# Kernel tuning notes

Measured on AMD Instinct MI355X. Metric: run time of the kernel, lower is better.

Reference implementation:

```python
import jax, jax.numpy as jnp
import numpy as np

V, E, U = 32000, 256, 512  # vocab, embed dim, LSTM units
B, S = 16, 130             # batch, seq len


def lstm_layer(x, mask, k, r, b):
    """Keras LSTMCell semantics. x:[B,T,D], mask:[B,T]; gates order i,f,c,o."""
    h0 = jnp.zeros((x.shape[0], U), x.dtype)
    c0 = h0
    xs = jnp.swapaxes(x, 0, 1)      # [T,B,D]
    ms = jnp.swapaxes(mask, 0, 1)   # [T,B]

    def step(carry, inp):
        h, c = carry
        xt, mt = inp
        z = xt @ k + h @ r + b
        i, f, g, o = jnp.split(z, 4, axis=-1)
        i = jax.nn.sigmoid(i); f = jax.nn.sigmoid(f); o = jax.nn.sigmoid(o)
        cn = f * c + i * jnp.tanh(g)
        hn = o * jnp.tanh(cn)
        m = mt[:, None]
        hn = jnp.where(m, hn, h)  # masked steps carry previous state/output
        cn = jnp.where(m, cn, c)
        return (hn, cn), hn

    _, ys = jax.lax.scan(step, (h0, c0), (xs, ms))
    return jnp.swapaxes(ys, 0, 1)  # [B,T,U]


def stacked_lstm(x, mask, params):
    h = x
    for (k, r, b) in params:
        h = lstm_layer(h, mask, k, r, b)
    return h


def setup_inputs() -> dict:
    key = jax.random.key(0)
    ks = jax.random.split(key, 20)
    d = {}
    d["seqs"] = jax.random.randint(ks[0], (B, S), 0, V)
    d["emb"] = jax.random.normal(ks[1], (V, E), jnp.float32) * 0.01
    i = 2
    for pre in ("f", "b"):
        in_dims = [E, U]
        for l in range(2):
            d[f"{pre}k{l}"] = jax.random.normal(ks[i], (in_dims[l], 4 * U), jnp.float32) * 0.05; i += 1
            d[f"{pre}r{l}"] = jax.random.normal(ks[i], (U, 4 * U), jnp.float32) * 0.05; i += 1
            d[f"{pre}b{l}"] = jnp.zeros((4 * U,), jnp.float32)
    d["Wp"] = jax.random.normal(ks[i], (2 * U, V), jnp.float32) * 0.02
    d["bp"] = jnp.zeros((V,), jnp.float32)
    return d


def reference(seqs, emb, fk0, fr0, fb0, fk1, fr1, fb1, bk0, br0, bb0, bk1, br1, bb1, Wp, bp):
    mask = seqs != 0                 # mask_zero=True
    embedded = emb[seqs]             # [B,S,E]
    # forward LM over tokens 0..S-2
    f = stacked_lstm(embedded[:, :-1], mask[:, :-1], [(fk0, fr0, fb0), (fk1, fr1, fb1)])
    # backward LM over tokens 1..S-1 (go_backwards: scan reversed input)
    xb = embedded[:, 1:][:, ::-1]
    mb = mask[:, 1:][:, ::-1]
    b = stacked_lstm(xb, mb, [(bk0, br0, bb0), (bk1, br1, bb1)])
    b_rev = b[:, ::-1]               # tf.reverse -> chronological order
    o = jnp.concatenate([f[:, :-1], b_rev[:, 1:]], axis=-1)  # [B,S-2,2U]
    return o @ Wp + bp               # [B,S-2,V]
```

## Files before the change

kernel.cpp:

```cpp
#include <hip/hip_runtime.h>

typedef __attribute__((ext_vector_type(8))) short bf16x8;
typedef __attribute__((ext_vector_type(4))) float f32x4;

__device__ __forceinline__ unsigned short f2bf(float x){
  union { float f; unsigned u; } v; v.f = x;
  unsigned r = v.u + 0x7FFFu + ((v.u >> 16) & 1u);
  return (unsigned short)(r >> 16);
}

__device__ __forceinline__ float sigm(float x){
  return 1.f / (1.f + __builtin_amdgcn_exp2f(-1.44269504f * x));
}
__device__ __forceinline__ float tanhfast(float x){
  return 2.f / (1.f + __builtin_amdgcn_exp2f(-2.88539008f * x)) - 1.f;
}

#define BYPASS_ST_SHORT(base, val) \
  asm volatile("global_store_short %0, %1, off sc0 sc1" :: "v"(base), "v"(val))

__device__ __forceinline__ int ld_flag(const int* p){
  int v;
  asm volatile("global_load_dword %0, %1, off sc0 sc1\n\t"
               "s_waitcnt vmcnt(0)"
               : "=v"(v) : "v"(p) : "memory");
  return v;
}

__device__ __forceinline__ void gload_lds16(const void* g, void* l){
  __builtin_amdgcn_global_load_lds(
      (const __attribute__((address_space(1))) unsigned*)g,
      (__attribute__((address_space(3))) unsigned*)l, 16, 0, 0);
}

__global__ void embed_kernel(const int* __restrict__ seqs, const float* __restrict__ emb,
                             unsigned short* __restrict__ x, int* __restrict__ mask,
                             int* __restrict__ flags){
  const int t = blockIdx.x, b = blockIdx.y, l = threadIdx.x;
  if (t == 0 && b == 0){
    #pragma unroll
    for (int j = 0; j < 16; ++j) flags[l + j*64] = 0;
  }
  const int tok = seqs[b*130 + t];
  if (l == 0) mask[b*130 + t] = (tok != 0) ? 1 : 0;
  const float* src = emb + (size_t)tok * 256;
  unsigned short* dst = x + ((size_t)b*130 + t)*256;
  #pragma unroll
  for (int j = 0; j < 4; ++j) dst[l + j*64] = f2bf(src[l + j*64]);
}

__global__ __launch_bounds__(512) void prep_transpose(
    const float* __restrict__ Wp,  unsigned short* __restrict__ WpT,
    const float* __restrict__ fk0, unsigned short* __restrict__ fk0T,
    const float* __restrict__ fr0, unsigned short* __restrict__ fr0T,
    const float* __restrict__ fk1, unsigned short* __restrict__ fk1T,
    const float* __restrict__ fr1, unsigned short* __restrict__ fr1T,
    const float* __restrict__ bk0, unsigned short* __restrict__ bk0T,
    const float* __restrict__ br0, unsigned short* __restrict__ br0T,
    const float* __restrict__ bk1, unsigned short* __restrict__ bk1T,
    const float* __restrict__ br1, unsigned short* __restrict__ br1T)
{
  __shared__ float tf[32*65];
  const int tid = threadIdx.x;
  const int tx = tid & 63, ty = tid >> 6;
  const int orow = tid & 31, oc = tid >> 5;
  for (int tile = blockIdx.x; tile < 19584; tile += gridDim.x){
    const float* src; unsigned short* dst; int R, C, r0, c0;
    if (tile < 16000){
      src = Wp; dst = WpT; R = 1024; C = 32000;
      const int kt = tile / 500, nt = tile - kt*500;
      r0 = kt*32; c0 = nt*64;
    } else {
      int u = tile - 16000;
      C = 2048;
      if (u < 256)      { src = fk0; dst = fk0T; R = 256;           }
      else if (u < 768) { src = fr0; dst = fr0T; R = 512; u -= 256; }
      else if (u < 1280){ src = fk1; dst = fk1T; R = 512; u -= 768; }
      else if (u < 1792){ src = fr1; dst = fr1T; R = 512; u -= 1280;}
      else if (u < 2048){ src = bk0; dst = bk0T; R = 256; u -= 1792;}
      else if (u < 2560){ src = br0; dst = br0T; R = 512; u -= 2048;}
      else if (u < 3072){ src = bk1; dst = bk1T; R = 512; u -= 2560;}
      else              { src = br1; dst = br1T; R = 512; u -= 3072;}
      const int kt = u >> 5, nt = u & 31;
      r0 = kt*32; c0 = nt*64;
    }
    #pragma unroll
    for (int j = 0; j < 4; ++j)
      tf[(ty + 8*j)*65 + tx] = src[(size_t)(r0 + ty + 8*j)*C + c0 + tx];
    __syncthreads();
    #pragma unroll
    for (int j = 0; j < 4; ++j)
      dst[(size_t)(c0 + oc + 16*j)*R + r0 + orow] = f2bf(tf[orow*65 + oc + 16*j]);
    __syncthreads();
  }
}

__global__ __launch_bounds__(512, 2) void lstm_coop(
    const unsigned short* __restrict__ x, const int* __restrict__ maskg,
    const unsigned short* __restrict__ fk0T, const unsigned short* __restrict__ fr0T,
    const unsigned short* __restrict__ fk1T, const unsigned short* __restrict__ fr1T,
    const unsigned short* __restrict__ bk0T, const unsigned short* __restrict__ br0T,
    const unsigned short* __restrict__ bk1T, const unsigned short* __restrict__ br1T,
    const float* __restrict__ fb0, const float* __restrict__ fb1,
    const float* __restrict__ bb0, const float* __restrict__ bb1,
    unsigned short* h0f, unsigned short* h0b,
    unsigned short* aproj, int* flags)
{
  const int wg = blockIdx.x;
  const int dir = wg >> 5;
  const int layer = (wg >> 4) & 1;
  const int u0 = (wg & 15) * 32;
  const int tid = threadIdx.x;
  const int w = tid >> 6, l = tid & 63;
  const int gate = w >> 1, half = w & 1;
  const int lr = l & 15, lk = l >> 4;
  const int cglob = gate*512 + u0 + half*16 + lr;

  const unsigned short* kT = (layer == 0) ? (dir ? bk0T : fk0T) : (dir ? bk1T : fk1T);
  const unsigned short* rT = (layer == 0) ? (dir ? br0T : fr0T) : (dir ? br1T : fr1T);
  const float* bias = (layer == 0) ? (dir ? bb0 : fb0) : (dir ? bb1 : fb1);
  unsigned short* h0 = dir ? h0b : h0f;

  int* fown  = flags + (layer*2 + dir)*256;
  int* fprod = flags + dir*256;
  int* fself = fown + (wg & 15)*16;

  bf16x8 wreg[16], kreg[16];
  #pragma unroll
  for (int i = 0; i < 16; ++i)
    wreg[i] = *(const bf16x8*)(rT + (size_t)cglob*512 + i*32 + lk*8);
  if (layer == 0){
    #pragma unroll
    for (int i = 0; i < 8; ++i)
      kreg[i] = *(const bf16x8*)(kT + (size_t)cglob*256 + i*32 + lk*8);
  } else {
    #pragma unroll
    for (int i = 0; i < 16; ++i)
      kreg[i] = *(const bf16x8*)(kT + (size_t)cglob*512 + i*32 + lk*8);
  }

  __shared__ float z_lds[4][16][32];
  __shared__ int mask_s[16*130];
  __shared__ __attribute__((aligned(16))) char h_lds[16*1024];
  __shared__ __attribute__((aligned(16))) char h2_lds[16*1024];
  for (int i = tid; i < 16*130; i += 512) mask_s[i] = maskg[i];

  float c_reg = 0.f, h_reg = 0.f;
  const int gu = tid & 31, gb = tid >> 5;
  const float bzi = bias[u0+gu], bzf = bias[512 + u0+gu];
  const float bzc = bias[1024 + u0+gu], bzo = bias[1536 + u0+gu];
  __syncthreads();

  for (int t = 0; t < 128; ++t){
    {
      const int* fp = nullptr; int tgt = 0;
      if (l < 16){ fp = fown + l*16; tgt = t; }
      else if (l < 32 && layer == 1){ fp = fprod + (l-16)*16; tgt = t + 1; }
      if (fp){
        while (ld_flag(fp) < tgt) __builtin_amdgcn_s_sleep(1);
      }
    }

    const int r0s = w*2;
    if (layer == 0){
      if (t > 0){
        #pragma unroll
        for (int j = 0; j < 2; ++j){
          const int r = r0s + j;
          const unsigned short* g = h0 + ((size_t)(t-1)*16 + r)*512 + ((l ^ (r & 7))*8);
          gload_lds16(g, h_lds + r*1024);
        }
      }
    } else {
      #pragma unroll
      for (int j = 0; j < 2; ++j){
        const int r = r0s + j;
        const unsigned short* g = h0 + ((size_t)t*16 + r)*512 + ((l ^ (r & 7))*8);
        gload_lds16(g, h_lds + r*1024);
      }
      if (t > 0){
        const int prow = dir ? (128 - t) : (t - 1);
        #pragma unroll
        for (int j = 0; j < 2; ++j){
          const int r = r0s + j;
          const unsigned short* g = aproj + ((size_t)(r*128 + prow))*1024 + dir*512 + ((l ^ (r & 7))*8);
          gload_lds16(g, h2_lds + r*1024);
        }
      }
    }

    f32x4 a0 = {0.f,0.f,0.f,0.f}, a1 = a0;
    const int fsw = (lr & 7) << 4;
    if (layer == 0){
      const int pos = dir ? (129 - t) : t;
      const unsigned short* xa = x + ((size_t)lr*130 + pos)*256 + lk*8;
      #pragma unroll
      for (int i = 0; i < 8; i += 2){
        bf16x8 va = *(const bf16x8*)(xa + i*32);
        bf16x8 vb = *(const bf16x8*)(xa + i*32 + 32);
        a0 = __builtin_amdgcn_mfma_f32_16x16x32_bf16(va, kreg[i],   a0, 0, 0, 0);
        a1 = __builtin_amdgcn_mfma_f32_16x16x32_bf16(vb, kreg[i+1], a1, 0, 0, 0);
      }
      if (t > 0){
        asm volatile("s_waitcnt vmcnt(0)" ::: "memory");
        __syncthreads();
        #pragma unroll
        for (int i = 0; i < 16; i += 2){
          bf16x8 v0 = *(const bf16x8*)(h_lds + lr*1024 + ((lk*16 + (i  )*64) ^ fsw));
          bf16x8 v1 = *(const bf16x8*)(h_lds + lr*1024 + ((lk*16 + (i+1)*64) ^ fsw));
          a0 = __builtin_amdgcn_mfma_f32_16x16x32_bf16(v0, wreg[i],   a0, 0, 0, 0);
          a1 = __builtin_amdgcn_mfma_f32_16x16x32_bf16(v1, wreg[i+1], a1, 0, 0, 0);
        }
      }
    } else {
      asm volatile("s_waitcnt vmcnt(0)" ::: "memory");
      __syncthreads();
      #pragma unroll
      for (int i = 0; i < 16; i += 2){
        bf16x8 v0 = *(const bf16x8*)(h_lds + lr*1024 + ((lk*16 + (i  )*64) ^ fsw));
        bf16x8 v1 = *(const bf16x8*)(h_lds + lr*1024 + ((lk*16 + (i+1)*64) ^ fsw));
        a0 = __builtin_amdgcn_mfma_f32_16x16x32_bf16(v0, kreg[i],   a0, 0, 0, 0);
        a1 = __builtin_amdgcn_mfma_f32_16x16x32_bf16(v1, kreg[i+1], a1, 0, 0, 0);
      }
      if (t > 0){
        #pragma unroll
        for (int i = 0; i < 16; i += 2){
          bf16x8 v0 = *(const bf16x8*)(h2_lds + lr*1024 + ((lk*16 + (i  )*64) ^ fsw));
          bf16x8 v1 = *(const bf16x8*)(h2_lds + lr*1024 + ((lk*16 + (i+1)*64) ^ fsw));
          a0 = __builtin_amdgcn_mfma_f32_16x16x32_bf16(v0, wreg[i],   a0, 0, 0, 0);
          a1 = __builtin_amdgcn_mfma_f32_16x16x32_bf16(v1, wreg[i+1], a1, 0, 0, 0);
        }
      }
    }
    {
      f32x4 acc = a0 + a1;
      #pragma unroll
      for (int r = 0; r < 4; ++r) z_lds[gate][lk*4 + r][half*16 + lr] = acc[r];
    }
    __syncthreads();

    {
      const float zi = z_lds[0][gb][gu] + bzi;
      const float zf = z_lds[1][gb][gu] + bzf;
      const float zc = z_lds[2][gb][gu] + bzc;
      const float zo = z_lds[3][gb][gu] + bzo;
      const float iv = sigm(zi);
      const float fv = sigm(zf);
      const float ov = sigm(zo);
      const float gv = tanhfast(zc);
      float cn = fv*c_reg + iv*gv;
      float hn = ov*tanhfast(cn);
      const int pos = dir ? (129 - t) : t;
      if (mask_s[gb*130 + pos] == 0){ cn = c_reg; hn = h_reg; }
      c_reg = cn; h_reg = hn;
      const unsigned short hb = f2bf(hn);
      if (layer == 0){
        unsigned short* p = h0 + ((size_t)t*16 + gb)*512 + u0 + gu;
        BYPASS_ST_SHORT(p, (unsigned)hb);
      } else {
        const int row = dir ? (127 - t) : t;
        unsigned short* p = aproj + ((size_t)gb*128 + row)*1024 + dir*512 + u0 + gu;
        BYPASS_ST_SHORT(p, (unsigned)hb);
      }
    }
    asm volatile("s_waitcnt vmcnt(0)" ::: "memory");
    __syncthreads();
    if (tid == 0){
      int v = t + 1;
      asm volatile("global_store_dword %0, %1, off sc0 sc1" :: "v"(fself), "v"(v) : "memory");
    }
  }
}

__global__ __launch_bounds__(256) void gemm_bf16(
    const unsigned short* __restrict__ A, const unsigned short* __restrict__ Bt,
    const float* __restrict__ bias, float* __restrict__ C,
    int M, int N, int K)
{
  __shared__ unsigned short lA[3][128*32], lB[3][128*32];
  const int tid = threadIdx.x;
  const int w = tid >> 6, l = tid & 63;
  const int wr = w >> 1, wc = w & 1;
  const int lr = l & 15, lk = l >> 4;
  const int orig = blockIdx.x;
  const int logical = (orig & 7)*500 + (orig >> 3);
  const int mt = logical & 15;
  const int nt = logical >> 4;
  const int brow = mt * 128, bcol = nt * 128;

  const int base0 = w*2048;
  const int base1 = w*2048 + 1024;
  const int L0 = base0 + l*16, L1 = base1 + l*16;
  const int Lg0 = L0 ^ (((L0 >> 7) & 3) << 4);
  const int Lg1 = L1 ^ (((L1 >> 7) & 3) << 4);
  const int row0 = Lg0 >> 6, kb0 = Lg0 & 63;
  const int row1 = Lg1 >> 6, kb1 = Lg1 & 63;

  f32x4 acc[4][4] = {};

  #define STAGE_KT(kt_, bu_) do{ \
    const int k0_ = (kt_) * 32; \
    gload_lds16((const char*)(A + (size_t)(brow+row0)*K + k0_) + kb0, (char*)lA[bu_] + base0); \
    gload_lds16((const char*)(Bt + (size_t)(bcol+row0)*K + k0_) + kb0, (char*)lB[bu_] + base0); \
    gload_lds16((const char*)(A + (size_t)(brow+row1)*K + k0_) + kb1, (char*)lA[bu_] + base1); \
    gload_lds16((const char*)(Bt + (size_t)(bcol+row1)*K + k0_) + kb1, (char*)lB[bu_] + base1); \
  }while(0)

  STAGE_KT(0, 0);
  STAGE_KT(1, 1);
  asm volatile("s_waitcnt vmcnt(4)" ::: "memory");
  __syncthreads();

  for (int kt = 0; kt < 32; ++kt){
    const int bu = kt - (kt / 3) * 3;
    if (kt < 30){
      const int nb = (kt + 2) - ((kt + 2) / 3) * 3;
      STAGE_KT(kt + 2, nb);
    }
    bf16x8 af[4], bfr[4];
    #pragma unroll
    for (int m = 0; m < 4; ++m){
      const int L = (wr*64 + m*16 + lr)*64 + lk*16;
      const int sp = L ^ (((L >> 7) & 3) << 4);
      af[m] = *(const bf16x8*)((char*)lA[bu] + sp);
    }
    #pragma unroll
    for (int n = 0; n < 4; ++n){
      const int L = (wc*64 + n*16 + lr)*64 + lk*16;
      const int sp = L ^ (((L >> 7) & 3) << 4);
      bfr[n] = *(const bf16x8*)((char*)lB[bu] + sp);
    }
    #pragma unroll
    for (int m = 0; m < 4; ++m)
      #pragma unroll
      for (int n = 0; n < 4; ++n)
        acc[m][n] = __builtin_amdgcn_mfma_f32_16x16x32_bf16(af[m], bfr[n], acc[m][n], 0, 0, 0);
    if (kt < 31){
      if (kt < 30) asm volatile("s_waitcnt vmcnt(4)" ::: "memory");
      else         asm volatile("s_waitcnt vmcnt(0)" ::: "memory");
      __syncthreads();
    }
  }
  #undef STAGE_KT

  #pragma unroll
  for (int m = 0; m < 4; ++m){
    #pragma unroll
    for (int n = 0; n < 4; ++n){
      const int col = bcol + wc*64 + n*16 + lr;
      const float bv = bias[col];
      const int row0_ = brow + wr*64 + m*16 + lk*4;
      #pragma unroll
      for (int r = 0; r < 4; ++r)
        C[(size_t)(row0_ + r)*N + col] = acc[m][n][r] + bv;
    }
  }
}

extern "C" void kernel_launch(void* const* d_in, const int* in_sizes, int n_in,
                              void* d_out, int out_size, void* d_ws, size_t ws_size,
                              hipStream_t stream){
  (void)in_sizes; (void)n_in; (void)out_size; (void)ws_size;
  const int*   seqs = (const int*)d_in[0];
  const float* emb  = (const float*)d_in[1];
  const float* fk0  = (const float*)d_in[2];
  const float* fr0  = (const float*)d_in[3];
  const float* fb0  = (const float*)d_in[4];
  const float* fk1  = (const float*)d_in[5];
  const float* fr1  = (const float*)d_in[6];
  const float* fb1  = (const float*)d_in[7];
  const float* bk0  = (const float*)d_in[8];
  const float* br0  = (const float*)d_in[9];
  const float* bb0  = (const float*)d_in[10];
  const float* bk1  = (const float*)d_in[11];
  const float* br1  = (const float*)d_in[12];
  const float* bb1  = (const float*)d_in[13];
  const float* Wp   = (const float*)d_in[14];
  const float* bp   = (const float*)d_in[15];
  float* out = (float*)d_out;

  char* ws = (char*)d_ws;
  size_t off = 0;
  auto alloc = [&](size_t b){ size_t o = off; off += (b + 255) & ~(size_t)255; return o; };
  int* flags            = (int*)(ws + alloc(4096));
  unsigned short* x     = (unsigned short*)(ws + alloc((size_t)16*130*256*2));
  int* mask             = (int*)(ws + alloc((size_t)16*130*4));
  unsigned short* fk0T  = (unsigned short*)(ws + alloc((size_t)2048*256*2));
  unsigned short* fr0T  = (unsigned short*)(ws + alloc((size_t)2048*512*2));
  unsigned short* fk1T  = (unsigned short*)(ws + alloc((size_t)2048*512*2));
  unsigned short* fr1T  = (unsigned short*)(ws + alloc((size_t)2048*512*2));
  unsigned short* bk0T  = (unsigned short*)(ws + alloc((size_t)2048*256*2));
  unsigned short* br0T  = (unsigned short*)(ws + alloc((size_t)2048*512*2));
  unsigned short* bk1T  = (unsigned short*)(ws + alloc((size_t)2048*512*2));
  unsigned short* br1T  = (unsigned short*)(ws + alloc((size_t)2048*512*2));
  unsigned short* h0f   = (unsigned short*)(ws + alloc((size_t)128*16*512*2));
  unsigned short* h0b   = (unsigned short*)(ws + alloc((size_t)128*16*512*2));
  unsigned short* aproj = (unsigned short*)(ws + alloc((size_t)2048*1024*2));
  unsigned short* WpT   = (unsigned short*)(ws + alloc((size_t)32000*1024*2));

  embed_kernel<<<dim3(130,16), 64, 0, stream>>>(seqs, emb, x, mask, flags);

  prep_transpose<<<1024, 512, 0, stream>>>(Wp, WpT,
      fk0, fk0T, fr0, fr0T, fk1, fk1T, fr1, fr1T,
      bk0, bk0T, br0, br0T, bk1, bk1T, br1, br1T);

  lstm_coop<<<64, 512, 0, stream>>>(x, mask,
      fk0T, fr0T, fk1T, fr1T, bk0T, br0T, bk1T, br1T,
      fb0, fb1, bb0, bb1, h0f, h0b, aproj, flags);

  gemm_bf16<<<4000, 256, 0, stream>>>(aproj, WpT, bp, out, 2048, 32000, 1024);
}
```

Measured before the change: 833.8 us.

## Overlap Wp transpose with LSTM recurrence using extra blocks in coop kernel

Moves the large Wp fp32->bf16 transpose out of the prep kernel and into 96 extra workgroups launched alongside the 64 LSTM workgroups, so the transpose runs concurrently with the latency-bound recurrence instead of before it. The prep kernel now handles only the small LSTM weight matrices. The risk is that the transpose blocks compete with the LSTM blocks for memory bandwidth and CU slots, and could delay the spin-waiting cooperative blocks if they are not co-resident.

```diff
diff --git a/kernel.cpp b/kernel.cpp
--- a/kernel.cpp
+++ b/kernel.cpp
@@ -49,8 +49,7 @@
   for (int j = 0; j < 4; ++j) dst[l + j*64] = f2bf(src[l + j*64]);
 }
 
-__global__ __launch_bounds__(512) void prep_transpose(
-    const float* __restrict__ Wp,  unsigned short* __restrict__ WpT,
+__global__ __launch_bounds__(512) void prep_small(
     const float* __restrict__ fk0, unsigned short* __restrict__ fk0T,
     const float* __restrict__ fr0, unsigned short* __restrict__ fr0T,
     const float* __restrict__ fk1, unsigned short* __restrict__ fk1T,
@@ -64,29 +63,22 @@
   const int tid = threadIdx.x;
   const int tx = tid & 63, ty = tid >> 6;
   const int orow = tid & 31, oc = tid >> 5;
-  for (int tile = blockIdx.x; tile < 19584; tile += gridDim.x){
-    const float* src; unsigned short* dst; int R, C, r0, c0;
-    if (tile < 16000){
-      src = Wp; dst = WpT; R = 1024; C = 32000;
-      const int kt = tile / 500, nt = tile - kt*500;
-      r0 = kt*32; c0 = nt*64;
-    } else {
-      int u = tile - 16000;
-      C = 2048;
-      if (u < 256)      { src = fk0; dst = fk0T; R = 256;           }
-      else if (u < 768) { src = fr0; dst = fr0T; R = 512; u -= 256; }
-      else if (u < 1280){ src = fk1; dst = fk1T; R = 512; u -= 768; }
-      else if (u < 1792){ src = fr1; dst = fr1T; R = 512; u -= 1280;}
-      else if (u < 2048){ src = bk0; dst = bk0T; R = 256; u -= 1792;}
-      else if (u < 2560){ src = br0; dst = br0T; R = 512; u -= 2048;}
-      else if (u < 3072){ src = bk1; dst = bk1T; R = 512; u -= 2560;}
-      else              { src = br1; dst = br1T; R = 512; u -= 3072;}
-      const int kt = u >> 5, nt = u & 31;
-      r0 = kt*32; c0 = nt*64;
-    }
+  for (int tile = blockIdx.x; tile < 3584; tile += gridDim.x){
+    const float* src; unsigned short* dst; int R, r0, c0;
+    int u = tile;
+    if (u < 256)      { src = fk0; dst = fk0T; R = 256;           }
+    else if (u < 768) { src = fr0; dst = fr0T; R = 512; u -= 256; }
+    else if (u < 1280){ src = fk1; dst = fk1T; R = 512; u -= 768; }
+    else if (u < 1792){ src = fr1; dst = fr1T; R = 512; u -= 1280;}
+    else if (u < 2048){ src = bk0; dst = bk0T; R = 256; u -= 1792;}
+    else if (u < 2560){ src = br0; dst = br0T; R = 512; u -= 2048;}
+    else if (u < 3072){ src = bk1; dst = bk1T; R = 512; u -= 2560;}
+    else              { src = br1; dst = br1T; R = 512; u -= 3072;}
+    const int kt = u >> 5, nt = u & 31;
+    r0 = kt*32; c0 = nt*64;
     #pragma unroll
     for (int j = 0; j < 4; ++j)
-      tf[(ty + 8*j)*65 + tx] = src[(size_t)(r0 + ty + 8*j)*C + c0 + tx];
+      tf[(ty + 8*j)*65 + tx] = src[(size_t)(r0 + ty + 8*j)*2048 + c0 + tx];
     __syncthreads();
     #pragma unroll
     for (int j = 0; j < 4; ++j)
@@ -103,14 +95,41 @@
     const unsigned short* __restrict__ bk1T, const unsigned short* __restrict__ br1T,
     const float* __restrict__ fb0, const float* __restrict__ fb1,
     const float* __restrict__ bb0, const float* __restrict__ bb1,
+    const float* __restrict__ Wp, unsigned short* __restrict__ WpT,
     unsigned short* h0f, unsigned short* h0b,
     unsigned short* aproj, int* flags)
 {
   const int wg = blockIdx.x;
+  const int tid = threadIdx.x;
+
+  __shared__ float z_lds[4][16][32];
+  __shared__ int mask_s[16*130];
+  __shared__ __attribute__((aligned(16))) char h_lds[16*1024];
+  __shared__ __attribute__((aligned(16))) char h2_lds[16*1024];
+
+  if (wg >= 64){
+    float* tf = (float*)h_lds;
+    const int tw = wg - 64;
+    const int tx = tid & 63, ty = tid >> 6;
+    const int orow = tid & 31, oc = tid >> 5;
+    for (int tile = tw; tile < 16000; tile += 96){
+      const int kt = tile / 500, nt = tile - kt*500;
+      const int r0 = kt*32, c0 = nt*64;
+      #pragma unroll
+      for (int j = 0; j < 4; ++j)
+        tf[(ty + 8*j)*65 + tx] = Wp[(size_t)(r0 + ty + 8*j)*32000 + c0 + tx];
+      __syncthreads();
+      #pragma unroll
+      for (int j = 0; j < 4; ++j)
+        WpT[(size_t)(c0 + oc + 16*j)*1024 + r0 + orow] = f2bf(tf[orow*65 + oc + 16*j]);
+      __syncthreads();
+    }
+    return;
+  }
+
   const int dir = wg >> 5;
   const int layer = (wg >> 4) & 1;
   const int u0 = (wg & 15) * 32;
-  const int tid = threadIdx.x;
   const int w = tid >> 6, l = tid & 63;
   const int gate = w >> 1, half = w & 1;
   const int lr = l & 15, lk = l >> 4;
@@ -139,10 +158,6 @@
       kreg[i] = *(const bf16x8*)(kT + (size_t)cglob*512 + i*32 + lk*8);
   }
 
-  __shared__ float z_lds[4][16][32];
-  __shared__ int mask_s[16*130];
-  __shared__ __attribute__((aligned(16))) char h_lds[16*1024];
-  __shared__ __attribute__((aligned(16))) char h2_lds[16*1024];
   for (int i = tid; i < 16*130; i += 512) mask_s[i] = maskg[i];
 
   float c_reg = 0.f, h_reg = 0.f;
@@ -400,13 +415,13 @@
 
   embed_kernel<<<dim3(130,16), 64, 0, stream>>>(seqs, emb, x, mask, flags);
 
-  prep_transpose<<<1024, 512, 0, stream>>>(Wp, WpT,
+  prep_small<<<256, 512, 0, stream>>>(
       fk0, fk0T, fr0, fr0T, fk1, fk1T, fr1, fr1T,
       bk0, bk0T, br0, br0T, bk1, bk1T, br1, br1T);
 
-  lstm_coop<<<64, 512, 0, stream>>>(x, mask,
+  lstm_coop<<<160, 512, 0, stream>>>(x, mask,
       fk0T, fr0T, fk1T, fr1T, bk0T, br0T, bk1T, br1T,
-      fb0, fb1, bb0, bb1, h0f, h0b, aproj, flags);
+      fb0, fb1, bb0, bb1, Wp, WpT, h0f, h0b, aproj, flags);
 
   gemm_bf16<<<4000, 256, 0, stream>>>(aproj, WpT, bp, out, 2048, 32000, 1024);
 }
```

After: 799.7 us. 1.04x faster.
